# Kernel tuning notes

Hardware: AMD Instinct MI355X
Metric: run time of the kernel (lower is better)

## Reference

```python
import jax, jax.numpy as jnp
import numpy as np

K = 56          # kernel_size (attended axis length)
HEADS = 8
IN_C = 64
OUT_C = 64
DH = OUT_C // HEADS  # 8; q,k use DH//2=4 channels, v uses DH=8
F_QR = 0.1
F_KR = 0.1
F_SVE = 0.1
F_SV = 1.0
EPS = 1e-5


def _bn(x, g, b, axes):
    # batch-norm in training mode: batch statistics over `axes`, affine per channel dim 1
    m = jnp.mean(x, axes, keepdims=True)
    v = jnp.var(x, axes, keepdims=True)
    shp = [1] * x.ndim
    shp[1] = -1
    return (x - m) * jax.lax.rsqrt(v + EPS) * g.reshape(shp) + b.reshape(shp)


def setup_inputs() -> dict:
    key = jax.random.key(0)
    ks = jax.random.split(key, 3)
    x = jax.random.normal(ks[0], (1, IN_C, 32, 56, K), dtype=jnp.float32)
    w_qkv = jax.random.normal(ks[1], (2 * OUT_C, IN_C), dtype=jnp.float32) * np.sqrt(1.0 / IN_C)
    relative = jax.random.normal(ks[2], (2 * DH, 2 * K - 1), dtype=jnp.float32) * np.sqrt(1.0 / DH)
    return {
        "x": x,
        "w_qkv": w_qkv,
        "relative": relative,
        "bn_qkv_g": jnp.ones((2 * OUT_C,), jnp.float32),
        "bn_qkv_b": jnp.zeros((2 * OUT_C,), jnp.float32),
        "bn_sim_g": jnp.ones((3 * HEADS,), jnp.float32),
        "bn_sim_b": jnp.zeros((3 * HEADS,), jnp.float32),
        "bn_out_g": jnp.ones((2 * OUT_C,), jnp.float32),
        "bn_out_b": jnp.zeros((2 * OUT_C,), jnp.float32),
    }


def reference(x, w_qkv, relative, bn_qkv_g, bn_qkv_b, bn_sim_g, bn_sim_b, bn_out_g, bn_out_b):
    N, C, D, Hdim, Wdim = x.shape  # axial='width': attend over W == K
    xp = jnp.transpose(x, (0, 2, 3, 1, 4)).reshape(N * D * Hdim, C, Wdim)  # (B, C, K)
    # 1x1 conv1d (no bias) + BN1d
    qkv = jnp.einsum("bci,oc->boi", xp, w_qkv)
    qkv = _bn(qkv, bn_qkv_g, bn_qkv_b, (0, 2))
    qkv = qkv.reshape(-1, HEADS, 2 * DH, K)
    q = qkv[:, :, : DH // 2]
    k = qkv[:, :, DH // 2 : DH]
    v = qkv[:, :, DH:]
    # relative position embeddings: emb[c,i,j] = relative[c, i - j + K - 1]
    idx = jnp.arange(K)
    rel_idx = idx[:, None] - idx[None, :] + K - 1  # (K, K)
    emb = relative[:, rel_idx]  # (2*DH, K, K)
    q_e, k_e, v_e = emb[: DH // 2], emb[DH // 2 : DH], emb[DH:]
    qr = jnp.einsum("bgci,cij->bgij", q, q_e) * F_QR
    kr = jnp.transpose(jnp.einsum("bgci,cij->bgij", k, k_e), (0, 1, 3, 2)) * F_KR
    qk = jnp.einsum("bgci,bgcj->bgij", q, k)
    stacked = jnp.concatenate([qk, qr, kr], axis=1)  # (B, 3*heads, K, K)
    stacked = _bn(stacked, bn_sim_g, bn_sim_b, (0, 2, 3))
    sim = jax.nn.softmax(stacked.reshape(-1, 3, HEADS, K, K).sum(axis=1), axis=3)
    sv = jnp.einsum("bgij,bgcj->bgci", sim, v) * F_SV
    sve = jnp.einsum("bgij,cij->bgci", sim, v_e) * F_SVE
    so = jnp.concatenate([sv, sve], axis=-1).reshape(-1, 2 * OUT_C, K)
    so = _bn(so, bn_out_g, bn_out_b, (0, 2))
    out = so.reshape(N, D, Hdim, OUT_C, 2, K).sum(axis=4)
    return jnp.transpose(out, (0, 3, 1, 2, 4))  # back to (N, OUT_C, D, H, W)
```

## Files before the change

### kernel.cpp

```cpp
#include <hip/hip_runtime.h>
#include <math.h>

typedef float v2f __attribute__((ext_vector_type(2)));

constexpr int KW      = 56;
constexpr int NB      = 1792;
constexpr int QKV_CH  = 128;
constexpr int SIM_CH  = 24;
constexpr int SLOTS   = 64;
constexpr int SMASK   = 63;
constexpr float EPS   = 1e-5f;

constexpr int   PA[10]  = {0,0,0,0,1,1,1,2,2,3};
constexpr int   PB[10]  = {0,1,2,3,1,2,3,2,3,3};
constexpr float PMf[10] = {1,2,2,2,1,2,2,1,2,1};

#if __has_builtin(__builtin_amdgcn_exp2f)
#define EXP2(x) __builtin_amdgcn_exp2f(x)
#else
#define EXP2(x) __expf((x) * 0.6931471805599453f)
#endif

__global__ __launch_bounds__(256) void k_qkv(const float* __restrict__ x,
                                             const float* __restrict__ w,
                                             const float* __restrict__ rel,
                                             float* __restrict__ qkv,
                                             float* __restrict__ sums,
                                             float* __restrict__ tabs) {
    const int t = threadIdx.x;
    if (blockIdx.x >= NB) {
        const int t0 = (blockIdx.x - NB) * 256 + t;
        const int STR = 8 * 256;
        float* Rq  = tabs;
        float* Rk  = tabs + 224;
        float* E2q = tabs + 448;
        float* E2k = tabs + 1008;
        float4* TQF = (float4*)(tabs + 1568);
        float4* TVF = (float4*)(tabs + 2464);
        for (int idx = t0; idx < 448; idx += STR) {
            int which = idx / 224, r = idx % 224;
            int i = r >> 2, c = r & 3;
            const float* src = rel + (which * 4 + c) * 111;
            float s = 0.f;
            for (int tt = 0; tt < 56; ++tt) s += src[i + tt];
            (which ? Rk : Rq)[r] = s;
        }
        for (int idx = t0; idx < 1120; idx += STR) {
            int which = idx / 560, r = idx % 560;
            int i = r / 10, p = r % 10;
            const float* sa = rel + (which * 4 + PA[p]) * 111;
            const float* sb = rel + (which * 4 + PB[p]) * 111;
            float s = 0.f;
            for (int tt = 0; tt < 56; ++tt) s += sa[i + tt] * sb[i + tt];
            (which ? E2k : E2q)[r] = s;
        }
        for (int d = t0; d < 112; d += STR) {
            bool v = d < 111;
            float4 tq, tk, ta, tb;
            tq.x = v ? rel[0 * 111 + d] : 0.f;
            tq.y = v ? rel[1 * 111 + d] : 0.f;
            tq.z = v ? rel[2 * 111 + d] : 0.f;
            tq.w = v ? rel[3 * 111 + d] : 0.f;
            tk.x = v ? rel[4 * 111 + 110 - d] : 0.f;
            tk.y = v ? rel[5 * 111 + 110 - d] : 0.f;
            tk.z = v ? rel[6 * 111 + 110 - d] : 0.f;
            tk.w = v ? rel[7 * 111 + 110 - d] : 0.f;
            ta.x = v ? rel[8 * 111 + d] : 0.f;
            ta.y = v ? rel[9 * 111 + d] : 0.f;
            ta.z = v ? rel[10 * 111 + d] : 0.f;
            ta.w = v ? rel[11 * 111 + d] : 0.f;
            tb.x = v ? rel[12 * 111 + d] : 0.f;
            tb.y = v ? rel[13 * 111 + d] : 0.f;
            tb.z = v ? rel[14 * 111 + d] : 0.f;
            tb.w = v ? rel[15 * 111 + d] : 0.f;
            TQF[d]       = tq;
            TQF[112 + d] = tk;
            TVF[d]       = ta;
            TVF[112 + d] = tb;
        }
        return;
    }
    __shared__ float xs[64 * KW];
    __shared__ float wt[64 * 128];
    __shared__ float s1[128], s2[128];
    const int b = blockIdx.x;

    if (t < 128) { s1[t] = 0.f; s2[t] = 0.f; }
    for (int idx = t; idx < 896; idx += 256) {
        int c = idx / 14, r = idx % 14;
        float4 v = *(const float4*)&x[c * 100352 + b * 56 + r * 4];
        *(float4*)&xs[c * 56 + r * 4] = v;
    }
    for (int idx = t; idx < 2048; idx += 256) {
        int o = idx >> 4, cq = idx & 15;
        float4 v = *(const float4*)&w[o * 64 + cq * 4];
        wt[(cq * 4 + 0) * 128 + o] = v.x;
        wt[(cq * 4 + 1) * 128 + o] = v.y;
        wt[(cq * 4 + 2) * 128 + o] = v.z;
        wt[(cq * 4 + 3) * 128 + o] = v.w;
    }
    __syncthreads();

    if (t < 224) {
        const int ob = t & 31, ib = t >> 5;
        v2f acc[4][4];
#pragma unroll
        for (int o = 0; o < 4; ++o)
#pragma unroll
            for (int ip = 0; ip < 4; ++ip) acc[o][ip] = (v2f)(0.f);
        for (int c = 0; c < 64; ++c) {
            float4 wv = *(const float4*)&wt[c * 128 + (ob << 2)];
            float4 x0 = *(const float4*)&xs[c * 56 + (ib << 3)];
            float4 x1 = *(const float4*)&xs[c * 56 + (ib << 3) + 4];
            v2f xp[4];
            xp[0] = (v2f){x0.x, x0.y}; xp[1] = (v2f){x0.z, x0.w};
            xp[2] = (v2f){x1.x, x1.y}; xp[3] = (v2f){x1.z, x1.w};
            v2f wd[4];
            wd[0] = (v2f)(wv.x); wd[1] = (v2f)(wv.y);
            wd[2] = (v2f)(wv.z); wd[3] = (v2f)(wv.w);
#pragma unroll
            for (int o = 0; o < 4; ++o)
#pragma unroll
                for (int ip = 0; ip < 4; ++ip)
                    acc[o][ip] += wd[o] * xp[ip];
        }
#pragma unroll
        for (int i = 0; i < 8; ++i) {
            float4 st;
            st.x = acc[0][i >> 1][i & 1];
            st.y = acc[1][i >> 1][i & 1];
            st.z = acc[2][i >> 1][i & 1];
            st.w = acc[3][i >> 1][i & 1];
            *(float4*)&qkv[b * 7168 + (ib * 8 + i) * 128 + ob * 4] = st;
        }
#pragma unroll
        for (int o = 0; o < 4; ++o) {
            float ps = 0.f, ps2 = 0.f;
#pragma unroll
            for (int ip = 0; ip < 4; ++ip) {
                ps  += acc[o][ip].x + acc[o][ip].y;
                ps2 += acc[o][ip].x * acc[o][ip].x + acc[o][ip].y * acc[o][ip].y;
            }
            atomicAdd(&s1[ob * 4 + o], ps);
            atomicAdd(&s2[ob * 4 + o], ps2);
        }
    }
    __syncthreads();
    if (t < 128) {
        float* dst = sums + (b & SMASK) * 256;
        atomicAdd(&dst[t], s1[t]);
        atomicAdd(&dst[128 + t], s2[t]);
    }
}

__global__ void k_coef(const float* __restrict__ sums, const float* __restrict__ g,
                       const float* __restrict__ bb, float* __restrict__ coef,
                       int nch, float invM) {
    const int o = blockIdx.x;
    const int s = threadIdx.x;
    float a1 = sums[s * 2 * nch + o];
    float a2 = sums[s * 2 * nch + nch + o];
#pragma unroll
    for (int mk = 1; mk < 64; mk <<= 1) {
        a1 += __shfl_xor(a1, mk);
        a2 += __shfl_xor(a2, mk);
    }
    if (s == 0) {
        float mean = a1 * invM;
        float var  = fmaxf(a2 * invM - mean * mean, 0.f);
        float sc   = g[o] * rsqrtf(var + EPS);
        coef[o] = sc;
        coef[nch + o] = bb[o] - mean * sc;
    }
}

__global__ __launch_bounds__(256) void k_simstats(const float* __restrict__ qkv,
                                                  const float* __restrict__ qcoef,
                                                  const float* __restrict__ Rq,
                                                  const float* __restrict__ Rk,
                                                  const float* __restrict__ E2q,
                                                  const float* __restrict__ E2k,
                                                  float* __restrict__ ssum) {
    const int wid = threadIdx.x >> 6, lane = threadIdx.x & 63;
    const int unit = blockIdx.x * 4 + wid;
    const int b = unit >> 3, g = unit & 7;
    const int iL = lane < 56 ? lane : 55;
    const float valid = lane < 56 ? 1.f : 0.f;

    const float* row = qkv + b * 7168 + iL * 128 + g * 16;
    float4 q4 = *(const float4*)(row);
    float4 k4 = *(const float4*)(row + 4);
    const float4 aq = *(const float4*)&qcoef[g * 16];
    const float4 ak = *(const float4*)&qcoef[g * 16 + 4];
    const float4 cq = *(const float4*)&qcoef[QKV_CH + g * 16];
    const float4 ck = *(const float4*)&qcoef[QKV_CH + g * 16 + 4];
    float qv[4], kv[4];
    qv[0] = (q4.x * aq.x + cq.x) * valid;
    qv[1] = (q4.y * aq.y + cq.y) * valid;
    qv[2] = (q4.z * aq.z + cq.z) * valid;
    qv[3] = (q4.w * aq.w + cq.w) * valid;
    kv[0] = (k4.x * ak.x + ck.x) * valid;
    kv[1] = (k4.y * ak.y + ck.y) * valid;
    kv[2] = (k4.z * ak.z + ck.z) * valid;
    kv[3] = (k4.w * ak.w + ck.w) * valid;

    float4 rq = *(const float4*)&Rq[iL * 4];
    float4 rk = *(const float4*)&Rk[iL * 4];
    float e2q[10], e2k[10];
#pragma unroll
    for (int p = 0; p < 10; ++p) { e2q[p] = E2q[iL * 10 + p]; e2k[p] = E2k[iL * 10 + p]; }

    float red[32];
#pragma unroll
    for (int c = 0; c < 4; ++c) { red[c] = qv[c]; red[4 + c] = kv[c]; }
#pragma unroll
    for (int p = 0; p < 10; ++p) {
        red[8 + p]  = qv[PA[p]] * qv[PB[p]];
        red[18 + p] = kv[PA[p]] * kv[PB[p]];
    }
    {
        float rqa[4] = {rq.x, rq.y, rq.z, rq.w};
        float rka[4] = {rk.x, rk.y, rk.z, rk.w};
        float pq = 0.f, pk = 0.f, pq2 = 0.f, pk2 = 0.f;
#pragma unroll
        for (int c = 0; c < 4; ++c) { pq += qv[c] * rqa[c]; pk += kv[c] * rka[c]; }
#pragma unroll
        for (int p = 0; p < 10; ++p) {
            pq2 += PMf[p] * red[8 + p]  * e2q[p];
            pk2 += PMf[p] * red[18 + p] * e2k[p];
        }
        red[28] = pq; red[29] = pk; red[30] = pq2; red[31] = pk2;
    }
#pragma unroll
    for (int v = 0; v < 32; ++v) {
        float xv = red[v];
#pragma unroll
        for (int mk = 1; mk < 64; mk <<= 1) xv += __shfl_xor(xv, mk);
        red[v] = xv;
    }
    float sqk = 0.f, sqk2 = 0.f;
#pragma unroll
    for (int c = 0; c < 4; ++c) sqk += red[c] * red[4 + c];
#pragma unroll
    for (int p = 0; p < 10; ++p) sqk2 += PMf[p] * red[8 + p] * red[18 + p];
    if (lane == 0) {
        float* ss = ssum + (blockIdx.x & SMASK) * 48;
        atomicAdd(&ss[g], sqk);
        atomicAdd(&ss[8 + g], 0.1f * red[28]);
        atomicAdd(&ss[16 + g], 0.1f * red[29]);
        atomicAdd(&ss[SIM_CH + g], sqk2);
        atomicAdd(&ss[SIM_CH + 8 + g], 0.01f * red[30]);
        atomicAdd(&ss[SIM_CH + 16 + g], 0.01f * red[31]);
    }
}

__global__ __launch_bounds__(256) void k_attn(const float* __restrict__ qkv,
                                              const float* __restrict__ qcoef,
                                              const float* __restrict__ scoef,
                                              const float4* __restrict__ TQF,
                                              const float4* __restrict__ TVF,
                                              float* __restrict__ sv2,
                                              float* __restrict__ sve2,
                                              float* __restrict__ osums) {
    __shared__ float4 TQs[224];
    __shared__ float4 TVs[224];
    __shared__ float4 KVs[4 * 168];
    __shared__ float Lsum[128];
    const int t = threadIdx.x;
    const int wid = t >> 6, lane = t & 63;
    const int unit = blockIdx.x * 4 + wid;
    const int b = unit >> 3, g = unit & 7;
    const int iL = lane < 56 ? lane : 55;

    if (t < 224) { TQs[t] = TQF[t]; TVs[t] = TVF[t]; }

    const float* row = qkv + b * 7168 + iL * 128 + g * 16;
    float4 q4  = *(const float4*)(row);
    float4 k4  = *(const float4*)(row + 4);
    float4 va4 = *(const float4*)(row + 8);
    float4 vb4 = *(const float4*)(row + 12);
    const float4 a0 = *(const float4*)&qcoef[g * 16];
    const float4 a1 = *(const float4*)&qcoef[g * 16 + 4];
    const float4 a2 = *(const float4*)&qcoef[g * 16 + 8];
    const float4 a3 = *(const float4*)&qcoef[g * 16 + 12];
    const float4 c0 = *(const float4*)&qcoef[QKV_CH + g * 16];
    const float4 c1 = *(const float4*)&qcoef[QKV_CH + g * 16 + 4];
    const float4 c2 = *(const float4*)&qcoef[QKV_CH + g * 16 + 8];
    const float4 c3 = *(const float4*)&qcoef[QKV_CH + g * 16 + 12];
    float4 kh, vh, wh;
    kh.x = k4.x * a1.x + c1.x;  kh.y = k4.y * a1.y + c1.y;
    kh.z = k4.z * a1.z + c1.z;  kh.w = k4.w * a1.w + c1.w;
    vh.x = va4.x * a2.x + c2.x; vh.y = va4.y * a2.y + c2.y;
    vh.z = va4.z * a2.z + c2.z; vh.w = va4.w * a2.w + c2.w;
    wh.x = vb4.x * a3.x + c3.x; wh.y = vb4.y * a3.y + c3.y;
    wh.z = vb4.z * a3.z + c3.z; wh.w = vb4.w * a3.w + c3.w;
    float qh[4];
    qh[0] = q4.x * a0.x + c0.x;  qh[1] = q4.y * a0.y + c0.y;
    qh[2] = q4.z * a0.z + c0.z;  qh[3] = q4.w * a0.w + c0.w;

    KVs[wid * 168 + iL]       = kh;
    KVs[wid * 168 + 56 + iL]  = vh;
    KVs[wid * 168 + 112 + iL] = wh;
    __syncthreads();

    const float L2E = 1.44269504088896340736f;
    const float aqk = scoef[g] * L2E;
    const float aqr = scoef[8 + g] * 0.1f * L2E;
    const float akr = scoef[16 + g] * 0.1f * L2E;
    const float cc2 = (scoef[SIM_CH + g] + scoef[SIM_CH + 8 + g]
                       + scoef[SIM_CH + 16 + g]) * L2E;
    const v2f qa01 = {qh[0] * aqk, qh[1] * aqk};
    const v2f qa23 = {qh[2] * aqk, qh[3] * aqk};
    const v2f qr01 = {qh[0] * aqr, qh[1] * aqr};
    const v2f qr23 = {qh[2] * aqr, qh[3] * aqr};
    const v2f akrp = {akr, akr};

    float l = 0.f;
    v2f sva = (v2f)(0.f), svb = (v2f)(0.f), svc = (v2f)(0.f), svd = (v2f)(0.f);
    v2f sea = (v2f)(0.f), seb = (v2f)(0.f), sec = (v2f)(0.f), sed = (v2f)(0.f);

    const float4* tqp = TQs + 55 + iL;
    const float4* tvp = TVs + 55 + iL;
    const float4* kvp = KVs + wid * 168;

#pragma unroll 4
    for (int j = 0; j < 56; ++j) {
        float4 tq = tqp[-j];
        float4 tk = tqp[112 - j];
        float4 ta = tvp[-j];
        float4 tb = tvp[112 - j];
        float4 kj = kvp[j];
        float4 vj = kvp[56 + j];
        float4 wj = kvp[112 + j];
        v2f u01 = akrp * (v2f){tk.x, tk.y} + qa01;
        v2f u23 = akrp * (v2f){tk.z, tk.w} + qa23;
        v2f acc = u01 * (v2f){kj.x, kj.y};
        acc += u23 * (v2f){kj.z, kj.w};
        acc += qr01 * (v2f){tq.x, tq.y};
        acc += qr23 * (v2f){tq.z, tq.w};
        float e = EXP2(acc.x + acc.y + cc2);
        l += e;
        v2f ep = {e, e};
        sva += ep * (v2f){vj.x, vj.y};
        svb += ep * (v2f){vj.z, vj.w};
        svc += ep * (v2f){wj.x, wj.y};
        svd += ep * (v2f){wj.z, wj.w};
        sea += ep * (v2f){ta.x, ta.y};
        seb += ep * (v2f){ta.z, ta.w};
        sec += ep * (v2f){tb.x, tb.y};
        sed += ep * (v2f){tb.z, tb.w};
    }
    const float inv = 1.f / l;
    const float inv1 = 0.1f * inv;
    float osv[8], ose[8];
    osv[0] = sva.x * inv;  osv[1] = sva.y * inv;
    osv[2] = svb.x * inv;  osv[3] = svb.y * inv;
    osv[4] = svc.x * inv;  osv[5] = svc.y * inv;
    osv[6] = svd.x * inv;  osv[7] = svd.y * inv;
    ose[0] = sea.x * inv1; ose[1] = sea.y * inv1;
    ose[2] = seb.x * inv1; ose[3] = seb.y * inv1;
    ose[4] = sec.x * inv1; ose[5] = sec.y * inv1;
    ose[6] = sed.x * inv1; ose[7] = sed.y * inv1;

    if (lane < 56) {
        size_t base = ((size_t)(g * 8) * 1792 + b) * 56 + iL;
#pragma unroll
        for (int c = 0; c < 8; ++c) {
            sv2[base + (size_t)c * 100352]  = osv[c];
            sve2[base + (size_t)c * 100352] = ose[c];
        }
    }
    const float valid = lane < 56 ? 1.f : 0.f;
    float red[32];
#pragma unroll
    for (int c = 0; c < 8; ++c) {
        red[c]      = osv[c] * valid;
        red[8 + c]  = ose[c] * valid;
        red[16 + c] = osv[c] * osv[c] * valid;
        red[24 + c] = ose[c] * ose[c] * valid;
    }
#pragma unroll
    for (int v = 0; v < 32; ++v) {
        float xv = red[v];
#pragma unroll
        for (int mk = 1; mk < 64; mk <<= 1) xv += __shfl_xor(xv, mk);
        red[v] = xv;
    }
    if (lane == 0) {
#pragma unroll
        for (int v = 0; v < 32; ++v) Lsum[wid * 32 + v] = red[v];
    }
    __syncthreads();
    if (t < 128) {
        const int ws_ = t >> 5, v = t & 31;
        const int g_ = (blockIdx.x * 4 + ws_) & 7;
        const int addr = ((v >> 4) & 1) * 128 + g_ * 16 + 2 * (v & 7) + ((v >> 3) & 1);
        float* dst = osums + (blockIdx.x & SMASK) * 256;
        atomicAdd(&dst[addr], Lsum[t]);
    }
}

__global__ __launch_bounds__(256) void k_out(const float* __restrict__ sv2,
                                             const float* __restrict__ sve2,
                                             const float* __restrict__ ocoef,
                                             float* __restrict__ out) {
    int e4 = blockIdx.x * 256 + threadIdx.x;
    int i0 = e4 * 4;
    int oc = i0 / 100352;
    int o0 = 2 * oc;
    float A = ocoef[o0], B = ocoef[o0 + 1];
    float C = ocoef[QKV_CH + o0] + ocoef[QKV_CH + o0 + 1];
    float4 v0 = *(const float4*)&sv2[i0];
    float4 v1 = *(const float4*)&sve2[i0];
    float4 r;
    r.x = A * v0.x + B * v1.x + C;
    r.y = A * v0.y + B * v1.y + C;
    r.z = A * v0.z + B * v1.z + C;
    r.w = A * v0.w + B * v1.w + C;
    *(float4*)&out[i0] = r;
}

extern "C" void kernel_launch(void* const* d_in, const int* in_sizes, int n_in,
                              void* d_out, int out_size, void* d_ws, size_t ws_size,
                              hipStream_t stream) {
    const float* x     = (const float*)d_in[0];
    const float* wqkv  = (const float*)d_in[1];
    const float* rel   = (const float*)d_in[2];
    const float* g_qkv = (const float*)d_in[3];
    const float* b_qkv = (const float*)d_in[4];
    const float* g_sim = (const float*)d_in[5];
    const float* b_sim = (const float*)d_in[6];
    const float* g_out = (const float*)d_in[7];
    const float* b_out = (const float*)d_in[8];
    float* out = (float*)d_out;
    float* ws = (float*)d_ws;

    float* qkv_raw  = ws;
    float* sv2      = ws + 12845056;
    float* sve2     = ws + 19267584;
    float* stats    = ws + 25690112;
    float* sums_buf = stats;
    float* qkv_coef = stats + 16384;
    float* sim_coef = stats + 16640;
    float* out_coef = stats + 16688;
    float* tabs     = stats + 16944;
    float* Rq   = tabs;
    float* Rk   = tabs + 224;
    float* E2q  = tabs + 448;
    float* E2k  = tabs + 1008;
    float4* TQF = (float4*)(tabs + 1568);
    float4* TVF = (float4*)(tabs + 2464);

    hipMemsetAsync(sums_buf, 0, SLOTS * 256 * sizeof(float), stream);

    k_qkv<<<NB + 8, 256, 0, stream>>>(x, wqkv, rel, qkv_raw, sums_buf, tabs);
    k_coef<<<QKV_CH, 64, 0, stream>>>(sums_buf, g_qkv, b_qkv, qkv_coef, QKV_CH,
                                      1.0f / 100352.0f);
    hipMemsetAsync(sums_buf, 0, SLOTS * 48 * sizeof(float), stream);
    k_simstats<<<3584, 256, 0, stream>>>(qkv_raw, qkv_coef, Rq, Rk, E2q, E2k,
                                         sums_buf);
    k_coef<<<SIM_CH, 64, 0, stream>>>(sums_buf, g_sim, b_sim, sim_coef, SIM_CH,
                                      1.0f / 5619712.0f);
    hipMemsetAsync(sums_buf, 0, SLOTS * 256 * sizeof(float), stream);
    k_attn<<<3584, 256, 0, stream>>>(qkv_raw, qkv_coef, sim_coef, TQF, TVF,
                                     sv2, sve2, sums_buf);
    k_coef<<<QKV_CH, 64, 0, stream>>>(sums_buf, g_out, b_out, out_coef, QKV_CH,
                                      1.0f / 100352.0f);
    k_out<<<6272, 256, 0, stream>>>(sv2, sve2, out_coef, out);
}
```

Measured before the change: 266.6 us.

## Pack relative-position tables as bf16, pad weight LDS, use transposed shuffle reduction

Stores the relative-position embedding tables in bf16 pairs, halving the LDS footprint and the number of table loads per step in the attention inner loop, and reassociates the logit arithmetic. The weight tile in LDS is padded to a 132-float stride to avoid bank conflicts, and the 32-value wave reduction is replaced by a recursive-halving transposed shuffle that removes the shared-memory staging and the block barrier. The bf16 rounding of embedding values reduces accuracy of the qr/kr/sve terms.

```diff
diff --git a/kernel.cpp b/kernel.cpp
--- a/kernel.cpp
+++ b/kernel.cpp
@@ -20,6 +20,16 @@
 #else
 #define EXP2(x) __expf((x) * 0.6931471805599453f)
 #endif
+
+__device__ inline unsigned bfr(float f) {
+    unsigned u = __float_as_uint(f);
+    return (u + 0x7fffu + ((u >> 16) & 1u)) >> 16;
+}
+__device__ inline unsigned pk2(float a, float b) {
+    return bfr(a) | (bfr(b) << 16);
+}
+__device__ inline float blo(unsigned u) { return __uint_as_float(u << 16); }
+__device__ inline float bhi(unsigned u) { return __uint_as_float(u & 0xffff0000u); }
 
 __global__ __launch_bounds__(256) void k_qkv(const float* __restrict__ x,
                                              const float* __restrict__ w,
@@ -35,8 +45,8 @@
         float* Rk  = tabs + 224;
         float* E2q = tabs + 448;
         float* E2k = tabs + 1008;
-        float4* TQF = (float4*)(tabs + 1568);
-        float4* TVF = (float4*)(tabs + 2464);
+        uint4* TQB = (uint4*)(tabs + 1568);
+        uint4* TVB = (uint4*)(tabs + 2016);
         for (int idx = t0; idx < 448; idx += STR) {
             int which = idx / 224, r = idx % 224;
             int i = r >> 2, c = r & 3;
@@ -73,15 +83,15 @@
             tb.y = v ? rel[13 * 111 + d] : 0.f;
             tb.z = v ? rel[14 * 111 + d] : 0.f;
             tb.w = v ? rel[15 * 111 + d] : 0.f;
-            TQF[d]       = tq;
-            TQF[112 + d] = tk;
-            TVF[d]       = ta;
-            TVF[112 + d] = tb;
+            TQB[d] = make_uint4(pk2(tq.x, tq.y), pk2(tq.z, tq.w),
+                                pk2(tk.x, tk.y), pk2(tk.z, tk.w));
+            TVB[d] = make_uint4(pk2(ta.x, ta.y), pk2(ta.z, ta.w),
+                                pk2(tb.x, tb.y), pk2(tb.z, tb.w));
         }
         return;
     }
     __shared__ float xs[64 * KW];
-    __shared__ float wt[64 * 128];
+    __shared__ float wt[64 * 132];
     __shared__ float s1[128], s2[128];
     const int b = blockIdx.x;
 
@@ -94,10 +104,10 @@
     for (int idx = t; idx < 2048; idx += 256) {
         int o = idx >> 4, cq = idx & 15;
         float4 v = *(const float4*)&w[o * 64 + cq * 4];
-        wt[(cq * 4 + 0) * 128 + o] = v.x;
-        wt[(cq * 4 + 1) * 128 + o] = v.y;
-        wt[(cq * 4 + 2) * 128 + o] = v.z;
-        wt[(cq * 4 + 3) * 128 + o] = v.w;
+        wt[(cq * 4 + 0) * 132 + o] = v.x;
+        wt[(cq * 4 + 1) * 132 + o] = v.y;
+        wt[(cq * 4 + 2) * 132 + o] = v.z;
+        wt[(cq * 4 + 3) * 132 + o] = v.w;
     }
     __syncthreads();
 
@@ -109,7 +119,7 @@
 #pragma unroll
             for (int ip = 0; ip < 4; ++ip) acc[o][ip] = (v2f)(0.f);
         for (int c = 0; c < 64; ++c) {
-            float4 wv = *(const float4*)&wt[c * 128 + (ob << 2)];
+            float4 wv = *(const float4*)&wt[c * 132 + (ob << 2)];
             float4 x0 = *(const float4*)&xs[c * 56 + (ib << 3)];
             float4 x1 = *(const float4*)&xs[c * 56 + (ib << 3) + 4];
             v2f xp[4];
@@ -221,15 +231,15 @@
     {
         float rqa[4] = {rq.x, rq.y, rq.z, rq.w};
         float rka[4] = {rk.x, rk.y, rk.z, rk.w};
-        float pq = 0.f, pk = 0.f, pq2 = 0.f, pk2 = 0.f;
+        float pq = 0.f, pk = 0.f, pq2 = 0.f, pk2_ = 0.f;
 #pragma unroll
         for (int c = 0; c < 4; ++c) { pq += qv[c] * rqa[c]; pk += kv[c] * rka[c]; }
 #pragma unroll
         for (int p = 0; p < 10; ++p) {
             pq2 += PMf[p] * red[8 + p]  * e2q[p];
-            pk2 += PMf[p] * red[18 + p] * e2k[p];
-        }
-        red[28] = pq; red[29] = pk; red[30] = pq2; red[31] = pk2;
+            pk2_ += PMf[p] * red[18 + p] * e2k[p];
+        }
+        red[28] = pq; red[29] = pk; red[30] = pq2; red[31] = pk2_;
     }
 #pragma unroll
     for (int v = 0; v < 32; ++v) {
@@ -257,22 +267,22 @@
 __global__ __launch_bounds__(256) void k_attn(const float* __restrict__ qkv,
                                               const float* __restrict__ qcoef,
                                               const float* __restrict__ scoef,
-                                              const float4* __restrict__ TQF,
-                                              const float4* __restrict__ TVF,
+                                              const uint4* __restrict__ TQB,
+                                              const uint4* __restrict__ TVB,
                                               float* __restrict__ sv2,
                                               float* __restrict__ sve2,
                                               float* __restrict__ osums) {
-    __shared__ float4 TQs[224];
-    __shared__ float4 TVs[224];
+    __shared__ uint4 Tqk[112];
+    __shared__ uint4 Tvb[112];
     __shared__ float4 KVs[4 * 168];
-    __shared__ float Lsum[128];
     const int t = threadIdx.x;
     const int wid = t >> 6, lane = t & 63;
     const int unit = blockIdx.x * 4 + wid;
     const int b = unit >> 3, g = unit & 7;
     const int iL = lane < 56 ? lane : 55;
 
-    if (t < 224) { TQs[t] = TQF[t]; TVs[t] = TVF[t]; }
+    if (t < 112) Tqk[t] = TQB[t];
+    else if (t < 224) Tvb[t - 112] = TVB[t - 112];
 
     const float* row = qkv + b * 7168 + iL * 128 + g * 16;
     float4 q4  = *(const float4*)(row);
@@ -319,36 +329,37 @@
     v2f sva = (v2f)(0.f), svb = (v2f)(0.f), svc = (v2f)(0.f), svd = (v2f)(0.f);
     v2f sea = (v2f)(0.f), seb = (v2f)(0.f), sec = (v2f)(0.f), sed = (v2f)(0.f);
 
-    const float4* tqp = TQs + 55 + iL;
-    const float4* tvp = TVs + 55 + iL;
+    const uint4*  Ap  = Tqk + 55 + iL;
+    const uint4*  Bp  = Tvb + 55 + iL;
     const float4* kvp = KVs + wid * 168;
 
 #pragma unroll 4
     for (int j = 0; j < 56; ++j) {
-        float4 tq = tqp[-j];
-        float4 tk = tqp[112 - j];
-        float4 ta = tvp[-j];
-        float4 tb = tvp[112 - j];
+        uint4 A = Ap[-j];
+        uint4 B = Bp[-j];
         float4 kj = kvp[j];
         float4 vj = kvp[56 + j];
         float4 wj = kvp[112 + j];
-        v2f u01 = akrp * (v2f){tk.x, tk.y} + qa01;
-        v2f u23 = akrp * (v2f){tk.z, tk.w} + qa23;
-        v2f acc = u01 * (v2f){kj.x, kj.y};
-        acc += u23 * (v2f){kj.z, kj.w};
-        acc += qr01 * (v2f){tq.x, tq.y};
-        acc += qr23 * (v2f){tq.z, tq.w};
-        float e = EXP2(acc.x + acc.y + cc2);
+        v2f kj01 = {kj.x, kj.y}, kj23 = {kj.z, kj.w};
+        v2f tq01 = {blo(A.x), bhi(A.x)}, tq23 = {blo(A.y), bhi(A.y)};
+        v2f tk01 = {blo(A.z), bhi(A.z)}, tk23 = {blo(A.w), bhi(A.w)};
+        v2f kr = tk01 * kj01 + tk23 * kj23;
+        v2f s  = qa01 * kj01;
+        s += qa23 * kj23;
+        s += qr01 * tq01;
+        s += qr23 * tq23;
+        s += akrp * kr;
+        float e = EXP2(s.x + s.y + cc2);
         l += e;
         v2f ep = {e, e};
         sva += ep * (v2f){vj.x, vj.y};
         svb += ep * (v2f){vj.z, vj.w};
         svc += ep * (v2f){wj.x, wj.y};
         svd += ep * (v2f){wj.z, wj.w};
-        sea += ep * (v2f){ta.x, ta.y};
-        seb += ep * (v2f){ta.z, ta.w};
-        sec += ep * (v2f){tb.x, tb.y};
-        sed += ep * (v2f){tb.z, tb.w};
+        sea += ep * (v2f){blo(B.x), bhi(B.x)};
+        seb += ep * (v2f){blo(B.y), bhi(B.y)};
+        sec += ep * (v2f){blo(B.z), bhi(B.z)};
+        sed += ep * (v2f){blo(B.w), bhi(B.w)};
     }
     const float inv = 1.f / l;
     const float inv1 = 0.1f * inv;
@@ -380,23 +391,24 @@
         red[24 + c] = ose[c] * ose[c] * valid;
     }
 #pragma unroll
-    for (int v = 0; v < 32; ++v) {
-        float xv = red[v];
-#pragma unroll
-        for (int mk = 1; mk < 64; mk <<= 1) xv += __shfl_xor(xv, mk);
-        red[v] = xv;
-    }
-    if (lane == 0) {
-#pragma unroll
-        for (int v = 0; v < 32; ++v) Lsum[wid * 32 + v] = red[v];
-    }
-    __syncthreads();
-    if (t < 128) {
-        const int ws_ = t >> 5, v = t & 31;
-        const int g_ = (blockIdx.x * 4 + ws_) & 7;
-        const int addr = ((v >> 4) & 1) * 128 + g_ * 16 + 2 * (v & 7) + ((v >> 3) & 1);
+    for (int k = 0; k < 5; ++k) {
+        const int m = 1 << k;
+        const int half = 16 >> k;
+        const bool up = (lane & m) != 0;
+#pragma unroll
+        for (int v = 0; v < half; ++v) {
+            float a = up ? red[v + half] : red[v];
+            float bsend = up ? red[v] : red[v + half];
+            red[v] = a + __shfl_xor(bsend, m);
+        }
+    }
+    red[0] += __shfl_xor(red[0], 32);
+    if (lane < 32) {
+        const int v = ((lane & 1) << 4) | ((lane & 2) << 2) | (lane & 4)
+                    | ((lane & 8) >> 2) | ((lane & 16) >> 4);
+        const int addr = ((v >> 4) & 1) * 128 + g * 16 + 2 * (v & 7) + ((v >> 3) & 1);
         float* dst = osums + (blockIdx.x & SMASK) * 256;
-        atomicAdd(&dst[addr], Lsum[t]);
+        atomicAdd(&dst[addr], red[0]);
     }
 }
 
@@ -448,8 +460,8 @@
     float* Rk   = tabs + 224;
     float* E2q  = tabs + 448;
     float* E2k  = tabs + 1008;
-    float4* TQF = (float4*)(tabs + 1568);
-    float4* TVF = (float4*)(tabs + 2464);
+    uint4* TQB  = (uint4*)(tabs + 1568);
+    uint4* TVB  = (uint4*)(tabs + 2016);
 
     hipMemsetAsync(sums_buf, 0, SLOTS * 256 * sizeof(float), stream);
 
@@ -462,7 +474,7 @@
     k_coef<<<SIM_CH, 64, 0, stream>>>(sums_buf, g_sim, b_sim, sim_coef, SIM_CH,
                                       1.0f / 5619712.0f);
     hipMemsetAsync(sums_buf, 0, SLOTS * 256 * sizeof(float), stream);
-    k_attn<<<3584, 256, 0, stream>>>(qkv_raw, qkv_coef, sim_coef, TQF, TVF,
+    k_attn<<<3584, 256, 0, stream>>>(qkv_raw, qkv_coef, sim_coef, TQB, TVB,
                                      sv2, sve2, sums_buf);
     k_coef<<<QKV_CH, 64, 0, stream>>>(sums_buf, g_out, b_out, out_coef, QKV_CH,
                                       1.0f / 100352.0f);
```

Measured after the change: 330.5 us. 24.0% more time.
